# Performance work log

Hardware: AMD Instinct MI355X
Metric: run time of the kernel (lower is better)

The kernel has to match this reference:

```python
import jax, jax.numpy as jnp
import numpy as np

TOKENS, IN_F, OUT_F = 8192, 4096, 16384


def setup_inputs() -> dict:
    key = jax.random.key(0)
    k1, k2, k3, k4, k5 = jax.random.split(key, 5)
    # int8-valued activations and weights (stored as int32; math identical)
    x = jax.random.randint(k1, (TOKENS, IN_F), -127, 128, dtype=jnp.int32)
    weight = jax.random.randint(k2, (OUT_F, IN_F), -127, 128, dtype=jnp.int32)
    # per-token activation scales and per-output-channel weight scales
    x_scales = jax.random.uniform(k3, (TOKENS,), jnp.float32, 1e-3, 2e-2)
    scales = jax.random.uniform(k4, (OUT_F,), jnp.float32, 1e-3, 2e-2)
    bias = jax.random.normal(k5, (OUT_F,), jnp.float32)
    return {"x": x, "weight": weight, "bias": bias, "x_scales": x_scales, "scales": scales}


def reference(x, weight, bias, x_scales, scales) -> jnp.ndarray:
    # q8_linear: int8 GEMM with int32 accumulation, then per-row (token) and
    # per-column (output channel) scale dequantization, fused bias add.
    # (Hadamard transform is applied at quantization time to both weights and
    # activations; in the dequantized domain it cancels, so the reference math
    # is the plain dequantized matmul.)
    acc = jnp.einsum("ti,oi->to", x, weight)  # int32 accumulate [T, O]
    out = acc.astype(jnp.float32) * x_scales[:, None] * scales[None, :]
    out = out + bias[None, :]
    return out
```

## Files before the change

### kernel.cpp

```cpp
#include <hip/hip_runtime.h>


#define T_DIM 8192
#define K_DIM 4096
#define N_DIM 16384

typedef __attribute__((ext_vector_type(4))) int int4v;

__global__ __launch_bounds__(256) void pack_i8(const int4v* __restrict__ src,
                                               int* __restrict__ dst) {
  const int idx = blockIdx.x * 256 + threadIdx.x;
  int4v v = src[idx];
  dst[idx] = (v.x & 255) | ((v.y & 255) << 8) | ((v.z & 255) << 16) | (v.w << 24);
}

__global__ __launch_bounds__(256) void gemm_i8(
    const char* __restrict__ A8,
    const char* __restrict__ B8,
    const float* __restrict__ xscale,
    const float* __restrict__ wscale,
    const float* __restrict__ bias,
    float* __restrict__ out) {
  __shared__ __align__(16) char lA[128 * 64];
  __shared__ __align__(16) char lB[128 * 64];

  const int tid = threadIdx.x;
  const int wave = tid >> 6;
  const int lane = tid & 63;
  const int blockM = blockIdx.y * 128;
  const int blockN = blockIdx.x * 128;
  const int waveM = (wave >> 1) * 64;
  const int waveN = (wave & 1) * 64;

  int4v acc[4][4] = {};

  const int srow = tid >> 2;
  const int scol = (tid & 3) << 4;
  const char* ag = A8 + (size_t)(blockM + srow) * K_DIM + scol;
  const char* bg = B8 + (size_t)(blockN + srow) * K_DIM + scol;
  char* lAdst = lA + wave * 1024;
  char* lBdst = lB + wave * 1024;

  const int q = lane >> 4;
  const int arow = waveM + (lane & 15);
  const int brow = waveN + (lane & 15);

  for (int k0 = 0; k0 < K_DIM; k0 += 64) {
    __syncthreads();
    __builtin_amdgcn_global_load_lds(
        (const __attribute__((address_space(1))) void*)(ag + k0),
        (__attribute__((address_space(3))) void*)(lAdst), 16, 0, 0);
    __builtin_amdgcn_global_load_lds(
        (const __attribute__((address_space(1))) void*)(ag + k0 + (size_t)64 * K_DIM),
        (__attribute__((address_space(3))) void*)(lAdst + 4096), 16, 0, 0);
    __builtin_amdgcn_global_load_lds(
        (const __attribute__((address_space(1))) void*)(bg + k0),
        (__attribute__((address_space(3))) void*)(lBdst), 16, 0, 0);
    __builtin_amdgcn_global_load_lds(
        (const __attribute__((address_space(1))) void*)(bg + k0 + (size_t)64 * K_DIM),
        (__attribute__((address_space(3))) void*)(lBdst + 4096), 16, 0, 0);
    __syncthreads();

    int4v afrag[4], bfrag[4];
#pragma unroll
    for (int i = 0; i < 4; ++i) {
      afrag[i] = *(const int4v*)(lA + ((arow + i * 16) * 64 + q * 16));
      bfrag[i] = *(const int4v*)(lB + ((brow + i * 16) * 64 + q * 16));
    }
#pragma unroll
    for (int im = 0; im < 4; ++im)
#pragma unroll
      for (int in = 0; in < 4; ++in)
        acc[im][in] = __builtin_amdgcn_mfma_i32_16x16x64_i8(
            afrag[im], bfrag[in], acc[im][in], 0, 0, 0);
  }

  const int row0 = blockM + waveM + q * 4;
  const int col0 = blockN + waveN + (lane & 15);
#pragma unroll
  for (int in = 0; in < 4; ++in) {
    const int o = col0 + in * 16;
    const float so = wscale[o];
    const float bo = bias[o];
#pragma unroll
    for (int im = 0; im < 4; ++im) {
      const int t = row0 + im * 16;
#pragma unroll
      for (int r = 0; r < 4; ++r) {
        const float v = (float)acc[im][in][r] * xscale[t + r] * so + bo;
        out[(size_t)(t + r) * N_DIM + o] = v;
      }
    }
  }
}

extern "C" void kernel_launch(void* const* d_in, const int* in_sizes, int n_in,
                              void* d_out, int out_size, void* d_ws, size_t ws_size,
                              hipStream_t stream) {
  const int* x = (const int*)d_in[0];
  const int* w = (const int*)d_in[1];
  const float* bias = (const float*)d_in[2];
  const float* xs = (const float*)d_in[3];
  const float* ws = (const float*)d_in[4];
  float* out = (float*)d_out;

  char* x8 = (char*)d_ws;
  char* w8 = x8 + (size_t)T_DIM * K_DIM;

  pack_i8<<<(T_DIM * K_DIM) / 1024, 256, 0, stream>>>((const int4v*)x, (int*)x8);
  pack_i8<<<(N_DIM / 4) * (K_DIM / 256), 256, 0, stream>>>((const int4v*)w, (int*)w8);

  dim3 grid(N_DIM / 128, T_DIM / 128);
  gemm_i8<<<grid, 256, 0, stream>>>(x8, w8, xs, ws, bias, out);
}
```

Measured before the change: 1.553 ms.

## Rewrite int8 GEMM with 256x256 tiles and a 4-stage LDS pipeline

Grows the block tile from 128x128 to 256x256 with 8 waves per block, each computing 128x64. Operands stream into a 4-buffer LDS ring via global_load_lds, with explicit vmcnt waits so loads run three tiles ahead of the MFMAs. LDS reads use an XOR swizzle to avoid bank conflicts, and block indices are remapped for L2 locality. MFMA phases run at raised priority between split barriers. The aim is more data reuse per byte loaded and hiding global-memory latency behind MFMA work. In exchange it uses much more LDS and more accumulator registers, which limits occupancy.

```diff
diff --git a/kernel.cpp b/kernel.cpp
--- a/kernel.cpp
+++ b/kernel.cpp
@@ -14,81 +14,147 @@
   dst[idx] = (v.x & 255) | ((v.y & 255) << 8) | ((v.z & 255) << 16) | (v.w << 24);
 }
 
-__global__ __launch_bounds__(256) void gemm_i8(
+__device__ __forceinline__ void gll16(const char* g, char* l) {
+  __builtin_amdgcn_global_load_lds(
+      (const __attribute__((address_space(1))) void*)g,
+      (__attribute__((address_space(3))) void*)l, 16, 0, 0);
+}
+
+#define MFMA_ROW(M, AF)                                                          \
+  acc[M][0] = __builtin_amdgcn_mfma_i32_16x16x64_i8(AF, b0, acc[M][0], 0, 0, 0); \
+  acc[M][1] = __builtin_amdgcn_mfma_i32_16x16x64_i8(AF, b1, acc[M][1], 0, 0, 0); \
+  acc[M][2] = __builtin_amdgcn_mfma_i32_16x16x64_i8(AF, b2, acc[M][2], 0, 0, 0); \
+  acc[M][3] = __builtin_amdgcn_mfma_i32_16x16x64_i8(AF, b3, acc[M][3], 0, 0, 0);
+
+#define VMW6 asm volatile("s_waitcnt vmcnt(6)" ::: "memory")
+#define VMW4 asm volatile("s_waitcnt vmcnt(4)" ::: "memory")
+#define VMW0 asm volatile("s_waitcnt vmcnt(0)" ::: "memory")
+
+#define TILE_BODY(KT, VMW, ST)                                                 \
+  do {                                                                         \
+    const int rbuf = (KT) & 3;                                                 \
+    const char* pa = &lA[rbuf][0] + aoff0;                                     \
+    const char* pb = &lB[rbuf][0] + boff0;                                     \
+              \
+    if (ST) {                                                                  \
+      const int sbuf = ((KT) + 3) & 3;                                         \
+      const size_t kc = (size_t)((KT) + 3) * 64;                               \
+      char* da = &lA[sbuf][tido];                                              \
+      gll16(sa + kc, da);                                                      \
+      gll16(sa + kc + (size_t)128 * K_DIM, da + 8192);                         \
+    }                                                                          \
+    VMW;                                                                       \
+    int4v a0 = *(const int4v*)(pa);                                            \
+    int4v a1 = *(const int4v*)(pa + 1024);                                     \
+    int4v a2 = *(const int4v*)(pa + 2048);                                     \
+    int4v a3 = *(const int4v*)(pa + 3072);                                     \
+    int4v b0 = *(const int4v*)(pb);                                            \
+    int4v b1 = *(const int4v*)(pb + 1024);                                     \
+    int4v b2 = *(const int4v*)(pb + 2048);                                     \
+    int4v b3 = *(const int4v*)(pb + 3072);                                     \
+    __builtin_amdgcn_s_barrier();                                              \
+    asm volatile("s_waitcnt lgkmcnt(0)" ::: "memory");                         \
+    __builtin_amdgcn_sched_barrier(0);                                         \
+    __builtin_amdgcn_s_setprio(1);                                             \
+    MFMA_ROW(0, a0) MFMA_ROW(1, a1) MFMA_ROW(2, a2) MFMA_ROW(3, a3)            \
+    __builtin_amdgcn_s_setprio(0);                                             \
+    __builtin_amdgcn_s_barrier();                                              \
+                   \
+    if (ST) {                                                                  \
+      const int sbuf = ((KT) + 3) & 3;                                         \
+      const size_t kc = (size_t)((KT) + 3) * 64;                               \
+      char* db = &lB[sbuf][tido];                                              \
+      gll16(sb + kc, db);                                                      \
+      gll16(sb + kc + (size_t)128 * K_DIM, db + 8192);                         \
+    }                                                                          \
+    int4v a4 = *(const int4v*)(pa + 4096);                                     \
+    int4v a5 = *(const int4v*)(pa + 5120);                                     \
+    int4v a6 = *(const int4v*)(pa + 6144);                                     \
+    int4v a7 = *(const int4v*)(pa + 7168);                                     \
+    __builtin_amdgcn_s_barrier();                                              \
+    asm volatile("s_waitcnt lgkmcnt(0)" ::: "memory");                         \
+    __builtin_amdgcn_sched_barrier(0);                                         \
+    __builtin_amdgcn_s_setprio(1);                                             \
+    MFMA_ROW(4, a4) MFMA_ROW(5, a5) MFMA_ROW(6, a6) MFMA_ROW(7, a7)            \
+    __builtin_amdgcn_s_setprio(0);                                             \
+    __builtin_amdgcn_s_barrier();                                              \
+  } while (0)
+
+__global__ __launch_bounds__(512, 2) void gemm_i8(
     const char* __restrict__ A8,
     const char* __restrict__ B8,
     const float* __restrict__ xscale,
     const float* __restrict__ wscale,
     const float* __restrict__ bias,
     float* __restrict__ out) {
-  __shared__ __align__(16) char lA[128 * 64];
-  __shared__ __align__(16) char lB[128 * 64];
+  __shared__ __align__(16) char lA[4][256 * 64];
+  __shared__ __align__(16) char lB[4][256 * 64];
 
   const int tid = threadIdx.x;
+  const int lane = tid & 63;
   const int wave = tid >> 6;
-  const int lane = tid & 63;
-  const int blockM = blockIdx.y * 128;
-  const int blockN = blockIdx.x * 128;
-  const int waveM = (wave >> 1) * 64;
-  const int waveN = (wave & 1) * 64;
+  const int mg = wave >> 2;
+  const int ng = wave & 3;
 
-  int4v acc[4][4] = {};
+  const int bid = blockIdx.x;
+  const int bx = (bid & 7) * 8 + ((bid >> 3) >> 5);
+  const int by = (bid >> 3) & 31;
+  const int blockM = by * 256;
+  const int blockN = bx * 256;
 
-  const int srow = tid >> 2;
-  const int scol = (tid & 3) << 4;
-  const char* ag = A8 + (size_t)(blockM + srow) * K_DIM + scol;
-  const char* bg = B8 + (size_t)(blockN + srow) * K_DIM + scol;
-  char* lAdst = lA + wave * 1024;
-  char* lBdst = lB + wave * 1024;
+  const int s2 = (tid & 7) ^ ((tid >> 3) & 7);
+  const int r0 = ((tid >> 3) << 1) | (s2 >> 2);
+  const int c0 = (s2 & 3) << 4;
+  const int tido = tid << 4;
+  const char* sa = A8 + (size_t)(blockM + r0) * K_DIM + c0;
+  const char* sb = B8 + (size_t)(blockN + r0) * K_DIM + c0;
 
+  const int ln = lane & 15;
   const int q = lane >> 4;
-  const int arow = waveM + (lane & 15);
-  const int brow = waveN + (lane & 15);
+  const int ra = mg * 128 + ln;
+  const int rbrow = ng * 64 + ln;
+  const int aoff0 =
+      ((ra >> 1) << 7) | (((((ra & 1) << 2) | q) ^ ((ra >> 1) & 7)) << 4);
+  const int boff0 =
+      ((rbrow >> 1) << 7) | (((((rbrow & 1) << 2) | q) ^ ((rbrow >> 1) & 7)) << 4);
 
-  for (int k0 = 0; k0 < K_DIM; k0 += 64) {
-    __syncthreads();
-    __builtin_amdgcn_global_load_lds(
-        (const __attribute__((address_space(1))) void*)(ag + k0),
-        (__attribute__((address_space(3))) void*)(lAdst), 16, 0, 0);
-    __builtin_amdgcn_global_load_lds(
-        (const __attribute__((address_space(1))) void*)(ag + k0 + (size_t)64 * K_DIM),
-        (__attribute__((address_space(3))) void*)(lAdst + 4096), 16, 0, 0);
-    __builtin_amdgcn_global_load_lds(
-        (const __attribute__((address_space(1))) void*)(bg + k0),
-        (__attribute__((address_space(3))) void*)(lBdst), 16, 0, 0);
-    __builtin_amdgcn_global_load_lds(
-        (const __attribute__((address_space(1))) void*)(bg + k0 + (size_t)64 * K_DIM),
-        (__attribute__((address_space(3))) void*)(lBdst + 4096), 16, 0, 0);
-    __syncthreads();
+  int4v acc[8][4] = {};
 
-    int4v afrag[4], bfrag[4];
 #pragma unroll
-    for (int i = 0; i < 4; ++i) {
-      afrag[i] = *(const int4v*)(lA + ((arow + i * 16) * 64 + q * 16));
-      bfrag[i] = *(const int4v*)(lB + ((brow + i * 16) * 64 + q * 16));
-    }
+  for (int t = 0; t < 3; ++t) {
+    const int kc = t * 64;
+    char* da = &lA[t][tido];
+    char* db = &lB[t][tido];
+    gll16(sa + kc, da);
+    gll16(sa + kc + (size_t)128 * K_DIM, da + 8192);
+    gll16(sb + kc, db);
+    gll16(sb + kc + (size_t)128 * K_DIM, db + 8192);
+  }
+  asm volatile("s_waitcnt vmcnt(8)" ::: "memory");
+  __builtin_amdgcn_s_barrier();
+
+#pragma unroll 1
+  for (int kt = 0; kt < 61; ++kt) {
+    TILE_BODY(kt, VMW6, 1);
+  }
+  TILE_BODY(61, VMW4, 0);
+  TILE_BODY(62, VMW0, 0);
+  TILE_BODY(63, VMW0, 0);
+
+  const int row0 = blockM + mg * 128 + q * 4;
+  const int col0 = blockN + ng * 64 + ln;
 #pragma unroll
-    for (int im = 0; im < 4; ++im)
-#pragma unroll
-      for (int in = 0; in < 4; ++in)
-        acc[im][in] = __builtin_amdgcn_mfma_i32_16x16x64_i8(
-            afrag[im], bfrag[in], acc[im][in], 0, 0, 0);
-  }
-
-  const int row0 = blockM + waveM + q * 4;
-  const int col0 = blockN + waveN + (lane & 15);
-#pragma unroll
-  for (int in = 0; in < 4; ++in) {
-    const int o = col0 + in * 16;
+  for (int n = 0; n < 4; ++n) {
+    const int o = col0 + n * 16;
     const float so = wscale[o];
     const float bo = bias[o];
 #pragma unroll
-    for (int im = 0; im < 4; ++im) {
-      const int t = row0 + im * 16;
+    for (int m = 0; m < 8; ++m) {
+      const int t = row0 + m * 16;
 #pragma unroll
       for (int r = 0; r < 4; ++r) {
-        const float v = (float)acc[im][in][r] * xscale[t + r] * so + bo;
-        out[(size_t)(t + r) * N_DIM + o] = v;
+        out[(size_t)(t + r) * N_DIM + o] =
+            (float)acc[m][n][r] * xscale[t + r] * so + bo;
       }
     }
   }
@@ -108,8 +174,7 @@
   char* w8 = x8 + (size_t)T_DIM * K_DIM;
 
   pack_i8<<<(T_DIM * K_DIM) / 1024, 256, 0, stream>>>((const int4v*)x, (int*)x8);
-  pack_i8<<<(N_DIM / 4) * (K_DIM / 256), 256, 0, stream>>>((const int4v*)w, (int*)w8);
+  pack_i8<<<((size_t)N_DIM * K_DIM) / 1024, 256, 0, stream>>>((const int4v*)w, (int*)w8);
 
-  dim3 grid(N_DIM / 128, T_DIM / 128);
-  gemm_i8<<<grid, 256, 0, stream>>>(x8, w8, xs, ws, bias, out);
+  gemm_i8<<<dim3(2048), 512, 0, stream>>>(x8, w8, xs, ws, bias, out);
 }
```

New measurement: 1.605 ms. 3.4% more time.
